# Kernel tuning notes

Measured on AMD Instinct MI355X. Metric: run time of the kernel, lower is better.

Reference implementation:

```python
import jax, jax.numpy as jnp
import numpy as np

N_ITER = 64   # projected-subgradient iterations of the batched DRO QP solver
LR0 = 0.05    # base step size (diminishing 1/sqrt(t))


def project_simplex(v):
    # Euclidean projection onto {z >= 0, sum z = 1} (sort-based, O(n log n))
    n = v.shape[0]
    u = jnp.sort(v)[::-1]
    css = jnp.cumsum(u) - 1.0
    k = jnp.arange(1, n + 1, dtype=v.dtype)
    cond = (u - css / k) > 0          # prefix-true pattern
    idx = jnp.sum(cond.astype(jnp.int32)) - 1
    theta = jnp.take(css, idx) / jnp.take(k, idx)
    return jnp.maximum(v - theta, 0.0)


def _dro_obj(z, c, lam, ep, y_hat, rho):
    # Tractable TV-DRO counterpart (Ben-Tal et al. 2013) with eta and obj_aux
    # eliminated analytically:
    #   obj_i* = max(-lam, u_i - eta),  u_i = (ep_i.z - c)^2
    #   feasibility: eta >= max_i u_i - lam; objective nondecreasing in eta
    #   => eta* = max_i u_i - lam
    s = ep @ z - c                     # (n_obs,)
    u = s * s
    umax = jnp.max(u)
    inner = jnp.mean(jnp.maximum(-lam, u - umax + lam))
    return (umax - lam) + rho * lam + inner - jnp.dot(y_hat, z)


_grad_obj = jax.grad(_dro_obj, argnums=(0, 1, 2))


def _solve_one(y_hat, ep, rho):
    # Projected subgradient descent on (z in simplex, c free, lam >= 0)
    n_y = y_hat.shape[0]
    z0 = jnp.full((n_y,), 1.0 / n_y, y_hat.dtype)
    c0 = jnp.mean(ep @ z0)
    lam0 = jnp.asarray(1.0, y_hat.dtype)

    def step(carry, t):
        z, c, lam = carry
        gz, gc, glam = _grad_obj(z, c, lam, ep, y_hat, rho)
        lr = LR0 / jnp.sqrt(t + 1.0)
        z = project_simplex(z - lr * gz)
        c = c - lr * gc
        lam = jnp.maximum(lam - lr * glam, 0.0)
        return (z, c, lam), None

    (z, _, _), _ = jax.lax.scan(step, (z0, c0, lam0),
                                jnp.arange(N_ITER, dtype=y_hat.dtype))
    return z


def setup_inputs() -> dict:
    key = jax.random.key(0)
    kx, ky, kw, kb = jax.random.split(key, 4)
    n_obs, n_x, n_y = 2048, 128, 64
    X = jax.random.normal(kx, (n_obs, n_x), jnp.float32)
    Y = jax.random.normal(ky, (n_obs, n_y), jnp.float32)
    W = jax.random.normal(kw, (n_y, n_x), jnp.float32) / np.sqrt(n_x).astype(np.float32)
    b = jax.random.normal(kb, (n_y,), jnp.float32) * 0.01
    rho = jnp.array([0.1], jnp.float32)
    return {"X": X, "Y": Y, "rho": rho, "W": W, "b": b}


def reference(X, Y, rho, W, b):
    # prediction layer: per-sample linear predict (vectorized over n_obs)
    Y_hat = X @ W.T + b                        # (n_obs, n_y)
    ep = Y - Y_hat                             # residuals, shared by all solves
    # batched DRO solve: one convex problem per scenario y_hat_t (vmapped)
    Z_star = jax.vmap(lambda yh: _solve_one(yh, ep, rho[0]))(Y_hat)
    Z_star = jax.lax.stop_gradient(Z_star)     # torch code detaches z_t
    return Z_star, Y_hat
```

## Files before the change

### kernel.cpp

```cpp
#include <hip/hip_runtime.h>

#define NOBS 2048
#define NX   128
#define NY   64
#define BS   8
#define NT   1024
#define NWAVE (NT / 64)
#define NITER 64

typedef short short8 __attribute__((ext_vector_type(8)));
typedef float f32x4 __attribute__((ext_vector_type(4)));

__device__ __forceinline__ unsigned short bf16_rne(float x) {
    unsigned u = __float_as_uint(x);
    return (unsigned short)((u + 0x7FFFu + ((u >> 16) & 1u)) >> 16);
}
__device__ __forceinline__ float bf16_tof(unsigned short h) {
    return __uint_as_float(((unsigned)h) << 16);
}

template <int CTRL>
__device__ __forceinline__ float dpp_f(float x) {
    return __int_as_float(__builtin_amdgcn_update_dpp(
        0, __float_as_int(x), CTRL, 0xf, 0xf, true));
}
__device__ __forceinline__ float wave_sum64(float v) {
    v += dpp_f<0x111>(v);
    v += dpp_f<0x112>(v);
    v += dpp_f<0x114>(v);
    v += dpp_f<0x118>(v);
    v += dpp_f<0x142>(v);
    v += dpp_f<0x143>(v);
    return v;
}
__device__ __forceinline__ float wave_max64_nonneg(float v) {
    v = fmaxf(v, dpp_f<0x111>(v));
    v = fmaxf(v, dpp_f<0x112>(v));
    v = fmaxf(v, dpp_f<0x114>(v));
    v = fmaxf(v, dpp_f<0x118>(v));
    v = fmaxf(v, dpp_f<0x142>(v));
    v = fmaxf(v, dpp_f<0x143>(v));
    return v;
}

__global__ __launch_bounds__(256) void prep_kernel(
    const float* __restrict__ X, const float* __restrict__ Y,
    const float* __restrict__ W, const float* __restrict__ b,
    float* __restrict__ yhat_out, float* __restrict__ ep, float* __restrict__ epsum,
    unsigned short* __restrict__ epT_hi, unsigned short* __restrict__ epT_lo)
{
    __shared__ float Xs[4][NX];
    const int t = threadIdx.x;
    const int row0 = blockIdx.x * 4;
    for (int f = t; f < 4 * NX; f += 256)
        Xs[f >> 7][f & 127] = X[(row0 + (f >> 7)) * NX + (f & 127)];
    __syncthreads();

    const int k = t & 63;
    const int r = t >> 6;
    const float4* W4 = reinterpret_cast<const float4*>(W + k * NX);
    const float4* X4 = reinterpret_cast<const float4*>(&Xs[r][0]);
    float acc = 0.f;
    #pragma unroll
    for (int x = 0; x < NX / 4; ++x) {
        float4 wv = W4[x];
        float4 xv = X4[x];
        acc += wv.x * xv.x + wv.y * xv.y + wv.z * xv.z + wv.w * xv.w;
    }
    const float yh = acc + b[k];
    const int i = row0 + r;
    yhat_out[i * NY + k] = yh;
    const float e = Y[i * NY + k] - yh;
    ep[i * NY + k] = e;

    {
        const unsigned short hi = bf16_rne(e);
        const unsigned short lo = bf16_rne(e - bf16_tof(hi));
        const int m  = k >> 4;
        const int q  = i >> 5;
        const int lc = (k & 15) + 16 * ((i >> 3) & 3);
        const int d  = i & 7;
        const int idx = ((m * 64 + q) * 64 + lc) * 8 + d;
        epT_hi[idx] = hi;
        epT_lo[idx] = lo;
    }

    float se = wave_sum64(e);
    if ((t & 63) == 63) atomicAdd(epsum, se);
}

__global__ __launch_bounds__(NT, 4) void solve_kernel(
    const float* __restrict__ ep, const float* __restrict__ yhat,
    const float* __restrict__ epsum, const float* __restrict__ rho_p,
    const unsigned short* __restrict__ epT_hi, const unsigned short* __restrict__ epT_lo,
    float* __restrict__ zout)
{
    __shared__ float Zs[BS][NY];
    __shared__ float Yh[BS][NY];
    __shared__ unsigned short VT_hi[BS][2056];
    __shared__ unsigned short VT_lo[BS][2056];
    __shared__ float Rp2[4][4][64][4];
    __shared__ float redM[NWAVE][BS];
    __shared__ float red2[NWAVE][4 * BS];
    __shared__ float cS[BS], lamS[BS];
    __shared__ __align__(16) unsigned short zb[8];

    const int t = threadIdx.x;
    const int lane = t & 63;
    const int wv = t >> 6;
    const int sc0 = blockIdx.x * BS;
    const float rho = rho_p[0];

    if (t < BS * NY) {
        const int j = t >> 6, k = t & 63;
        Yh[j][k] = yhat[(sc0 + j) * NY + k];
        Zs[j][k] = 1.0f / 64.0f;
    }
    if (t < BS) {
        cS[t] = epsum[0] * (1.0f / 131072.0f);
        lamS[t] = 1.0f;
    }
    if (t < 8) zb[t] = 0;
    __syncthreads();

    const int i0 = t;
    const int i1 = t + NT;
    const float4* ep4 = reinterpret_cast<const float4*>(ep);

    for (int it = 0; it < NITER; ++it) {
        const float lr = 0.05f / sqrtf((float)it + 1.0f);

        float s0[BS], s1[BS];
        #pragma unroll
        for (int j = 0; j < BS; ++j) { s0[j] = 0.f; s1[j] = 0.f; }
        #pragma unroll 4
        for (int k4 = 0; k4 < NY / 4; ++k4) {
            const float4 ea = ep4[i0 * (NY / 4) + k4];
            const float4 eb = ep4[i1 * (NY / 4) + k4];
            #pragma unroll
            for (int j = 0; j < BS; ++j) {
                const float4 zv = *reinterpret_cast<const float4*>(&Zs[j][k4 * 4]);
                s0[j] += ea.x * zv.x + ea.y * zv.y + ea.z * zv.z + ea.w * zv.w;
                s1[j] += eb.x * zv.x + eb.y * zv.y + eb.z * zv.z + eb.w * zv.w;
            }
        }
        float lamR[BS];
        #pragma unroll
        for (int j = 0; j < BS; ++j) {
            const float cj = cS[j];
            lamR[j] = lamS[j];
            s0[j] -= cj; s1[j] -= cj;
        }

        #pragma unroll
        for (int j = 0; j < BS; ++j) {
            float pm = fmaxf(s0[j] * s0[j], s1[j] * s1[j]);
            pm = wave_max64_nonneg(pm);
            if (lane == 63) redM[wv][j] = pm;
        }
        __syncthreads();

        float mv = 0.f;
        if (lane < BS) {
            #pragma unroll
            for (int w = 0; w < NWAVE; ++w) mv = fmaxf(mv, redM[w][lane]);
        }
        float umaxR[BS];
        #pragma unroll
        for (int j = 0; j < BS; ++j) umaxR[j] = __shfl(mv, j, 64);

        #pragma unroll
        for (int j = 0; j < BS; ++j) {
            const float um = umaxR[j], lm = lamR[j];
            float pa = 0.f, pe = 0.f, pas = 0.f, pes = 0.f;
            {
                const float s = s0[j], u = s * s;
                const float x = (u - um) + lm;
                const float a = (x > -lm) ? 1.0f : ((x == -lm) ? 0.5f : 0.0f);
                const float e = (u == um) ? 1.0f : 0.0f;
                pa += a; pe += e; pas += a * s; pes += e * s;
            }
            {
                const float s = s1[j], u = s * s;
                const float x = (u - um) + lm;
                const float a = (x > -lm) ? 1.0f : ((x == -lm) ? 0.5f : 0.0f);
                const float e = (u == um) ? 1.0f : 0.0f;
                pa += a; pe += e; pas += a * s; pes += e * s;
            }
            pa = wave_sum64(pa); pe = wave_sum64(pe);
            pas = wave_sum64(pas); pes = wave_sum64(pes);
            if (lane == 63) {
                red2[wv][j]          = pa;  red2[wv][BS + j]     = pe;
                red2[wv][2 * BS + j] = pas; red2[wv][3 * BS + j] = pes;
            }
        }
        __syncthreads();

        float sv = 0.f;
        if (lane < 4 * BS) {
            #pragma unroll
            for (int w = 0; w < NWAVE; ++w) sv += red2[w][lane];
        }
        float wAr[BS], gcKeep = 0.f, glamKeep = 0.f;
        #pragma unroll
        for (int j = 0; j < BS; ++j) {
            const float sumA   = __shfl(sv, j, 64);
            const float sumEq  = __shfl(sv, BS + j, 64);
            const float sumAS  = __shfl(sv, 2 * BS + j, 64);
            const float sumEqS = __shfl(sv, 3 * BS + j, 64);
            const float abar = sumA * (1.0f / (float)NOBS);
            const float wA = (1.0f - abar) / sumEq;
            wAr[j] = wA;
            if (lane == j) {
                gcKeep   = -2.0f * (sumAS * (1.0f / (float)NOBS) + wA * sumEqS);
                glamKeep = (rho - 2.0f) + 2.0f * abar;
            }
        }
        if (wv == 0 && lane < BS) {
            cS[lane]  = cS[lane] - lr * gcKeep;
            lamS[lane] = fmaxf(lamS[lane] - lr * glamKeep, 0.0f);
        }

        #pragma unroll
        for (int j = 0; j < BS; ++j) {
            const float um = umaxR[j], lm = lamR[j], wA = wAr[j];
            float v0j, v1j;
            {
                const float s = s0[j], u = s * s;
                const float x = (u - um) + lm;
                const float a = (x > -lm) ? 1.0f : ((x == -lm) ? 0.5f : 0.0f);
                const float e = (u == um) ? 1.0f : 0.0f;
                v0j = (a * (1.0f / (float)NOBS) + e * wA) * s;
            }
            {
                const float s = s1[j], u = s * s;
                const float x = (u - um) + lm;
                const float a = (x > -lm) ? 1.0f : ((x == -lm) ? 0.5f : 0.0f);
                const float e = (u == um) ? 1.0f : 0.0f;
                v1j = (a * (1.0f / (float)NOBS) + e * wA) * s;
            }
            const unsigned short h0 = bf16_rne(v0j);
            VT_hi[j][i0] = h0;
            VT_lo[j][i0] = bf16_rne(v0j - bf16_tof(h0));
            const unsigned short h1 = bf16_rne(v1j);
            VT_hi[j][i1] = h1;
            VT_lo[j][i1] = bf16_rne(v1j - bf16_tof(h1));
        }
        __syncthreads();

        {
            const int m = wv & 3;
            const int g = wv >> 2;
            const int jb = lane & 15;
            const int h  = lane >> 4;
            const bool jvalid = (jb < BS);
            f32x4 acc = {0.f, 0.f, 0.f, 0.f};
            #pragma unroll 4
            for (int qq = 0; qq < 16; ++qq) {
                const int q = g * 16 + qq;
                const int aoff = ((m * 64 + q) * 64 + lane) * 8;
                const short8 ah = *(const short8*)(epT_hi + aoff);
                const short8 al = *(const short8*)(epT_lo + aoff);
                const unsigned short* vh = jvalid ? &VT_hi[jb][(q << 5) + (h << 3)] : zb;
                const unsigned short* vl = jvalid ? &VT_lo[jb][(q << 5) + (h << 3)] : zb;
                const short8 bh = *(const short8*)vh;
                const short8 bl = *(const short8*)vl;
                acc = __builtin_amdgcn_mfma_f32_16x16x32_bf16(al, bh, acc, 0, 0, 0);
                acc = __builtin_amdgcn_mfma_f32_16x16x32_bf16(ah, bl, acc, 0, 0, 0);
                acc = __builtin_amdgcn_mfma_f32_16x16x32_bf16(ah, bh, acc, 0, 0, 0);
            }
            *(f32x4*)(&Rp2[g][m][lane][0]) = acc;
        }
        __syncthreads();

        if (wv < BS) {
            const int j = wv, k = lane;
            const int m = k >> 4, p = k & 3, ll = ((k >> 2) & 3) * 16 + j;
            const float r = Rp2[0][m][ll][p] + Rp2[1][m][ll][p]
                          + Rp2[2][m][ll][p] + Rp2[3][m][ll][p];
            const float gz = 2.0f * r - Yh[j][k];
            const float vz = Zs[j][k] - lr * gz;

            float sv2 = vz;
            #pragma unroll
            for (int sz = 2; sz <= 64; sz <<= 1) {
                #pragma unroll
                for (int st = sz >> 1; st > 0; st >>= 1) {
                    const float other = __shfl_xor(sv2, st, 64);
                    const bool desc = ((lane & sz) == 0);
                    const bool lower = ((lane & st) == 0);
                    const float mx = fmaxf(sv2, other), mn = fminf(sv2, other);
                    sv2 = (lower == desc) ? mx : mn;
                }
            }
            float css = sv2;
            #pragma unroll
            for (int off = 1; off < 64; off <<= 1) {
                const float nb = __shfl_up(css, off, 64);
                if (lane >= off) css += nb;
            }
            css -= 1.0f;
            const bool cond = (sv2 - css / (float)(lane + 1)) > 0.0f;
            const unsigned long long bal = __ballot(cond);
            const int idx = __popcll(bal) - 1;
            const float cssIdx = __shfl(css, idx, 64);
            const float theta = cssIdx / (float)(idx + 1);
            Zs[j][k] = fmaxf(vz - theta, 0.0f);
        }
        __syncthreads();
    }

    if (t < BS * NY) {
        const int j = t >> 6, k = t & 63;
        zout[(sc0 + j) * NY + k] = Zs[j][k];
    }
}

extern "C" void kernel_launch(void* const* d_in, const int* in_sizes, int n_in,
                              void* d_out, int out_size, void* d_ws, size_t ws_size,
                              hipStream_t stream) {
    const float* X   = (const float*)d_in[0];
    const float* Y   = (const float*)d_in[1];
    const float* rho = (const float*)d_in[2];
    const float* W   = (const float*)d_in[3];
    const float* b   = (const float*)d_in[4];

    float* out   = (float*)d_out;
    float* zout  = out;
    float* yhat  = out + NOBS * NY;

    unsigned short* epT_hi = (unsigned short*)d_ws;
    unsigned short* epT_lo = epT_hi + NY * NOBS;
    float* ep    = (float*)(epT_lo + NY * NOBS);
    float* epsum = ep + NOBS * NY;

    hipMemsetAsync(epsum, 0, sizeof(float), stream);
    prep_kernel<<<NOBS / 4, 256, 0, stream>>>(X, Y, W, b, yhat, ep, epsum, epT_hi, epT_lo);
    solve_kernel<<<NOBS / BS, NT, 0, stream>>>(ep, yhat, epsum, rho, epT_hi, epT_lo, zout);
}
```

Baseline: 1.892 ms.

## Compute forward residual products with triple-bf16 MFMA instead of scalar fp32 FMA

The forward product ep@z for all observations and 8 scenarios moves from scalar fp32 dot products over global float4 loads to bf16 MFMA. Residuals are split three ways (hi/md/lo) and z is split the same way, using six cross-term MFMAs to keep near-fp32 accuracy. The fp32 residual buffer goes away, and the reductions are reorganised around the MFMA output layout, using shuffles and vectorised VT writes. The cost is extra MFMA work on padded (duplicated) scenario columns, a third residual copy in memory, and a risk of small numerical drift that could change the argmax ties in the subgradient.

```diff
diff --git a/kernel.cpp b/kernel.cpp
--- a/kernel.cpp
+++ b/kernel.cpp
@@ -10,6 +10,7 @@
 
 typedef short short8 __attribute__((ext_vector_type(8)));
 typedef float f32x4 __attribute__((ext_vector_type(4)));
+typedef unsigned short u16x4 __attribute__((ext_vector_type(4)));
 
 __device__ __forceinline__ unsigned short bf16_rne(float x) {
     unsigned u = __float_as_uint(x);
@@ -33,21 +34,14 @@
     v += dpp_f<0x143>(v);
     return v;
 }
-__device__ __forceinline__ float wave_max64_nonneg(float v) {
-    v = fmaxf(v, dpp_f<0x111>(v));
-    v = fmaxf(v, dpp_f<0x112>(v));
-    v = fmaxf(v, dpp_f<0x114>(v));
-    v = fmaxf(v, dpp_f<0x118>(v));
-    v = fmaxf(v, dpp_f<0x142>(v));
-    v = fmaxf(v, dpp_f<0x143>(v));
-    return v;
-}
 
 __global__ __launch_bounds__(256) void prep_kernel(
     const float* __restrict__ X, const float* __restrict__ Y,
     const float* __restrict__ W, const float* __restrict__ b,
-    float* __restrict__ yhat_out, float* __restrict__ ep, float* __restrict__ epsum,
-    unsigned short* __restrict__ epT_hi, unsigned short* __restrict__ epT_lo)
+    float* __restrict__ yhat_out, float* __restrict__ epsum,
+    unsigned short* __restrict__ epT_hi, unsigned short* __restrict__ epT_lo,
+    unsigned short* __restrict__ epA_hi, unsigned short* __restrict__ epA_md,
+    unsigned short* __restrict__ epA_lo)
 {
     __shared__ float Xs[4][NX];
     const int t = threadIdx.x;
@@ -71,18 +65,29 @@
     const int i = row0 + r;
     yhat_out[i * NY + k] = yh;
     const float e = Y[i * NY + k] - yh;
-    ep[i * NY + k] = e;
-
+
+    const unsigned short hi = bf16_rne(e);
+    const float r1 = e - bf16_tof(hi);
+    const unsigned short md = bf16_rne(r1);
+    const unsigned short lo = bf16_rne(r1 - bf16_tof(md));
     {
-        const unsigned short hi = bf16_rne(e);
-        const unsigned short lo = bf16_rne(e - bf16_tof(hi));
         const int m  = k >> 4;
         const int q  = i >> 5;
         const int lc = (k & 15) + 16 * ((i >> 3) & 3);
         const int d  = i & 7;
         const int idx = ((m * 64 + q) * 64 + lc) * 8 + d;
         epT_hi[idx] = hi;
-        epT_lo[idx] = lo;
+        epT_lo[idx] = md;
+    }
+    {
+        const int m  = i >> 4;
+        const int q  = k >> 5;
+        const int lc = (i & 15) + 16 * ((k >> 3) & 3);
+        const int d  = k & 7;
+        const int idx = ((m * 2 + q) * 64 + lc) * 8 + d;
+        epA_hi[idx] = hi;
+        epA_md[idx] = md;
+        epA_lo[idx] = lo;
     }
 
     float se = wave_sum64(e);
@@ -90,24 +95,33 @@
 }
 
 __global__ __launch_bounds__(NT, 4) void solve_kernel(
-    const float* __restrict__ ep, const float* __restrict__ yhat,
-    const float* __restrict__ epsum, const float* __restrict__ rho_p,
+    const float* __restrict__ yhat, const float* __restrict__ epsum,
+    const float* __restrict__ rho_p,
     const unsigned short* __restrict__ epT_hi, const unsigned short* __restrict__ epT_lo,
+    const unsigned short* __restrict__ epA_hi, const unsigned short* __restrict__ epA_md,
+    const unsigned short* __restrict__ epA_lo,
     float* __restrict__ zout)
 {
     __shared__ float Zs[BS][NY];
     __shared__ float Yh[BS][NY];
     __shared__ unsigned short VT_hi[BS][2056];
     __shared__ unsigned short VT_lo[BS][2056];
+    __shared__ __align__(16) unsigned short Zb_hi[16][72];
+    __shared__ __align__(16) unsigned short Zb_md[16][72];
+    __shared__ __align__(16) unsigned short Zb_lo[16][72];
     __shared__ float Rp2[4][4][64][4];
     __shared__ float redM[NWAVE][BS];
-    __shared__ float red2[NWAVE][4 * BS];
-    __shared__ float cS[BS], lamS[BS];
+    __shared__ float red2[NWAVE][BS][4];
+    __shared__ float cS[16], lamS[16];
     __shared__ __align__(16) unsigned short zb[8];
 
     const int t = threadIdx.x;
     const int lane = t & 63;
     const int wv = t >> 6;
+    const int jb = lane & 15;
+    const int h  = lane >> 4;
+    const int j8 = jb & 7;
+    const bool hiHalf = (jb >= 8);
     const int sc0 = blockIdx.x * BS;
     const float rho = rho_p[0];
 
@@ -116,160 +130,147 @@
         Yh[j][k] = yhat[(sc0 + j) * NY + k];
         Zs[j][k] = 1.0f / 64.0f;
     }
-    if (t < BS) {
+    {
+        const int j = t >> 6, k = t & 63;
+        Zb_hi[j][k] = bf16_rne(1.0f / 64.0f);
+        Zb_md[j][k] = 0;
+        Zb_lo[j][k] = 0;
+    }
+    if (t < 16) {
         cS[t] = epsum[0] * (1.0f / 131072.0f);
         lamS[t] = 1.0f;
     }
     if (t < 8) zb[t] = 0;
     __syncthreads();
 
-    const int i0 = t;
-    const int i1 = t + NT;
-    const float4* ep4 = reinterpret_cast<const float4*>(ep);
-
     for (int it = 0; it < NITER; ++it) {
         const float lr = 0.05f / sqrtf((float)it + 1.0f);
 
-        float s0[BS], s1[BS];
-        #pragma unroll
-        for (int j = 0; j < BS; ++j) { s0[j] = 0.f; s1[j] = 0.f; }
-        #pragma unroll 4
-        for (int k4 = 0; k4 < NY / 4; ++k4) {
-            const float4 ea = ep4[i0 * (NY / 4) + k4];
-            const float4 eb = ep4[i1 * (NY / 4) + k4];
-            #pragma unroll
-            for (int j = 0; j < BS; ++j) {
-                const float4 zv = *reinterpret_cast<const float4*>(&Zs[j][k4 * 4]);
-                s0[j] += ea.x * zv.x + ea.y * zv.y + ea.z * zv.z + ea.w * zv.w;
-                s1[j] += eb.x * zv.x + eb.y * zv.y + eb.z * zv.z + eb.w * zv.w;
-            }
-        }
-        float lamR[BS];
-        #pragma unroll
-        for (int j = 0; j < BS; ++j) {
-            const float cj = cS[j];
-            lamR[j] = lamS[j];
-            s0[j] -= cj; s1[j] -= cj;
-        }
-
-        #pragma unroll
-        for (int j = 0; j < BS; ++j) {
-            float pm = fmaxf(s0[j] * s0[j], s1[j] * s1[j]);
-            pm = wave_max64_nonneg(pm);
-            if (lane == 63) redM[wv][j] = pm;
-        }
-        __syncthreads();
-
-        float mv = 0.f;
-        if (lane < BS) {
-            #pragma unroll
-            for (int w = 0; w < NWAVE; ++w) mv = fmaxf(mv, redM[w][lane]);
-        }
-        float umaxR[BS];
-        #pragma unroll
-        for (int j = 0; j < BS; ++j) umaxR[j] = __shfl(mv, j, 64);
-
-        #pragma unroll
-        for (int j = 0; j < BS; ++j) {
-            const float um = umaxR[j], lm = lamR[j];
-            float pa = 0.f, pe = 0.f, pas = 0.f, pes = 0.f;
-            {
-                const float s = s0[j], u = s * s;
+        f32x4 acc[8];
+        #pragma unroll
+        for (int mi = 0; mi < 8; ++mi) acc[mi] = (f32x4){0.f, 0.f, 0.f, 0.f};
+        #pragma unroll
+        for (int q = 0; q < 2; ++q) {
+            const short8 zh = *(const short8*)&Zb_hi[jb][(q << 5) + (h << 3)];
+            const short8 zm = *(const short8*)&Zb_md[jb][(q << 5) + (h << 3)];
+            const short8 zl = *(const short8*)&Zb_lo[jb][(q << 5) + (h << 3)];
+            #pragma unroll
+            for (int mi = 0; mi < 8; ++mi) {
+                const int aoff = ((((wv << 3) + mi) * 2 + q) * 64 + lane) * 8;
+                const short8 ah = *(const short8*)(epA_hi + aoff);
+                const short8 am = *(const short8*)(epA_md + aoff);
+                const short8 al = *(const short8*)(epA_lo + aoff);
+                acc[mi] = __builtin_amdgcn_mfma_f32_16x16x32_bf16(al, zh, acc[mi], 0, 0, 0);
+                acc[mi] = __builtin_amdgcn_mfma_f32_16x16x32_bf16(ah, zl, acc[mi], 0, 0, 0);
+                acc[mi] = __builtin_amdgcn_mfma_f32_16x16x32_bf16(am, zm, acc[mi], 0, 0, 0);
+                acc[mi] = __builtin_amdgcn_mfma_f32_16x16x32_bf16(am, zh, acc[mi], 0, 0, 0);
+                acc[mi] = __builtin_amdgcn_mfma_f32_16x16x32_bf16(ah, zm, acc[mi], 0, 0, 0);
+                acc[mi] = __builtin_amdgcn_mfma_f32_16x16x32_bf16(ah, zh, acc[mi], 0, 0, 0);
+            }
+        }
+        const float cR = cS[jb];
+        const float lm = lamS[jb];
+        float sv_[4][4], u_[4][4];
+        #pragma unroll
+        for (int n = 0; n < 4; ++n)
+            #pragma unroll
+            for (int p = 0; p < 4; ++p) {
+                const float av = hiHalf ? acc[n + 4][p] : acc[n][p];
+                const float ss = av - cR;
+                sv_[n][p] = ss;
+                u_[n][p] = ss * ss;
+            }
+
+        float pm = u_[0][0];
+        #pragma unroll
+        for (int n = 0; n < 4; ++n)
+            #pragma unroll
+            for (int p = 0; p < 4; ++p) pm = fmaxf(pm, u_[n][p]);
+        pm = fmaxf(pm, __shfl_xor(pm, 8, 64));
+        pm = fmaxf(pm, __shfl_xor(pm, 16, 64));
+        pm = fmaxf(pm, __shfl_xor(pm, 32, 64));
+        if (lane < 8) redM[wv][lane] = pm;
+        __syncthreads();
+
+        float um = redM[0][j8];
+        #pragma unroll
+        for (int w = 1; w < NWAVE; ++w) um = fmaxf(um, redM[w][j8]);
+
+        float pa = 0.f, pe = 0.f, pas = 0.f, pes = 0.f;
+        #pragma unroll
+        for (int n = 0; n < 4; ++n)
+            #pragma unroll
+            for (int p = 0; p < 4; ++p) {
+                const float ss = sv_[n][p], u = u_[n][p];
                 const float x = (u - um) + lm;
                 const float a = (x > -lm) ? 1.0f : ((x == -lm) ? 0.5f : 0.0f);
                 const float e = (u == um) ? 1.0f : 0.0f;
-                pa += a; pe += e; pas += a * s; pes += e * s;
-            }
-            {
-                const float s = s1[j], u = s * s;
+                pa += a; pe += e; pas += a * ss; pes += e * ss;
+            }
+        pa  += __shfl_xor(pa, 8, 64);  pa  += __shfl_xor(pa, 16, 64);  pa  += __shfl_xor(pa, 32, 64);
+        pe  += __shfl_xor(pe, 8, 64);  pe  += __shfl_xor(pe, 16, 64);  pe  += __shfl_xor(pe, 32, 64);
+        pas += __shfl_xor(pas, 8, 64); pas += __shfl_xor(pas, 16, 64); pas += __shfl_xor(pas, 32, 64);
+        pes += __shfl_xor(pes, 8, 64); pes += __shfl_xor(pes, 16, 64); pes += __shfl_xor(pes, 32, 64);
+        if (lane < 8) {
+            f32x4 r4 = {pa, pe, pas, pes};
+            *(f32x4*)&red2[wv][lane][0] = r4;
+        }
+        __syncthreads();
+
+        float sA = 0.f, sE = 0.f, sAS = 0.f, sES = 0.f;
+        #pragma unroll
+        for (int w = 0; w < NWAVE; ++w) {
+            const f32x4 rr = *(const f32x4*)&red2[w][j8][0];
+            sA += rr[0]; sE += rr[1]; sAS += rr[2]; sES += rr[3];
+        }
+        const float abar = sA * (1.0f / (float)NOBS);
+        const float wA = (1.0f - abar) / sE;
+        const float gc = -2.0f * (sAS * (1.0f / (float)NOBS) + wA * sES);
+        const float glam = (rho - 2.0f) + 2.0f * abar;
+        if (wv == 0 && lane < 16) {
+            cS[lane] = cS[lane] - lr * gc;
+            lamS[lane] = fmaxf(lamS[lane] - lr * glam, 0.0f);
+        }
+
+        #pragma unroll
+        for (int n = 0; n < 4; ++n) {
+            u16x4 vh4, vl4;
+            #pragma unroll
+            for (int p = 0; p < 4; ++p) {
+                const float ss = sv_[n][p], u = u_[n][p];
                 const float x = (u - um) + lm;
                 const float a = (x > -lm) ? 1.0f : ((x == -lm) ? 0.5f : 0.0f);
                 const float e = (u == um) ? 1.0f : 0.0f;
-                pa += a; pe += e; pas += a * s; pes += e * s;
-            }
-            pa = wave_sum64(pa); pe = wave_sum64(pe);
-            pas = wave_sum64(pas); pes = wave_sum64(pes);
-            if (lane == 63) {
-                red2[wv][j]          = pa;  red2[wv][BS + j]     = pe;
-                red2[wv][2 * BS + j] = pas; red2[wv][3 * BS + j] = pes;
-            }
-        }
-        __syncthreads();
-
-        float sv = 0.f;
-        if (lane < 4 * BS) {
-            #pragma unroll
-            for (int w = 0; w < NWAVE; ++w) sv += red2[w][lane];
-        }
-        float wAr[BS], gcKeep = 0.f, glamKeep = 0.f;
-        #pragma unroll
-        for (int j = 0; j < BS; ++j) {
-            const float sumA   = __shfl(sv, j, 64);
-            const float sumEq  = __shfl(sv, BS + j, 64);
-            const float sumAS  = __shfl(sv, 2 * BS + j, 64);
-            const float sumEqS = __shfl(sv, 3 * BS + j, 64);
-            const float abar = sumA * (1.0f / (float)NOBS);
-            const float wA = (1.0f - abar) / sumEq;
-            wAr[j] = wA;
-            if (lane == j) {
-                gcKeep   = -2.0f * (sumAS * (1.0f / (float)NOBS) + wA * sumEqS);
-                glamKeep = (rho - 2.0f) + 2.0f * abar;
-            }
-        }
-        if (wv == 0 && lane < BS) {
-            cS[lane]  = cS[lane] - lr * gcKeep;
-            lamS[lane] = fmaxf(lamS[lane] - lr * glamKeep, 0.0f);
-        }
-
-        #pragma unroll
-        for (int j = 0; j < BS; ++j) {
-            const float um = umaxR[j], lm = lamR[j], wA = wAr[j];
-            float v0j, v1j;
-            {
-                const float s = s0[j], u = s * s;
-                const float x = (u - um) + lm;
-                const float a = (x > -lm) ? 1.0f : ((x == -lm) ? 0.5f : 0.0f);
-                const float e = (u == um) ? 1.0f : 0.0f;
-                v0j = (a * (1.0f / (float)NOBS) + e * wA) * s;
-            }
-            {
-                const float s = s1[j], u = s * s;
-                const float x = (u - um) + lm;
-                const float a = (x > -lm) ? 1.0f : ((x == -lm) ? 0.5f : 0.0f);
-                const float e = (u == um) ? 1.0f : 0.0f;
-                v1j = (a * (1.0f / (float)NOBS) + e * wA) * s;
-            }
-            const unsigned short h0 = bf16_rne(v0j);
-            VT_hi[j][i0] = h0;
-            VT_lo[j][i0] = bf16_rne(v0j - bf16_tof(h0));
-            const unsigned short h1 = bf16_rne(v1j);
-            VT_hi[j][i1] = h1;
-            VT_lo[j][i1] = bf16_rne(v1j - bf16_tof(h1));
+                const float vv = (a * (1.0f / (float)NOBS) + e * wA) * ss;
+                const unsigned short vhh = bf16_rne(vv);
+                vh4[p] = vhh;
+                vl4[p] = bf16_rne(vv - bf16_tof(vhh));
+            }
+            const int ii = ((wv << 3) + (hiHalf ? 4 : 0) + n) * 16 + (h << 2);
+            *(u16x4*)&VT_hi[j8][ii] = vh4;
+            *(u16x4*)&VT_lo[j8][ii] = vl4;
         }
         __syncthreads();
 
         {
             const int m = wv & 3;
             const int g = wv >> 2;
-            const int jb = lane & 15;
-            const int h  = lane >> 4;
-            const bool jvalid = (jb < BS);
-            f32x4 acc = {0.f, 0.f, 0.f, 0.f};
+            f32x4 accC = {0.f, 0.f, 0.f, 0.f};
             #pragma unroll 4
             for (int qq = 0; qq < 16; ++qq) {
                 const int q = g * 16 + qq;
                 const int aoff = ((m * 64 + q) * 64 + lane) * 8;
                 const short8 ah = *(const short8*)(epT_hi + aoff);
                 const short8 al = *(const short8*)(epT_lo + aoff);
-                const unsigned short* vh = jvalid ? &VT_hi[jb][(q << 5) + (h << 3)] : zb;
-                const unsigned short* vl = jvalid ? &VT_lo[jb][(q << 5) + (h << 3)] : zb;
+                const unsigned short* vh = (!hiHalf) ? &VT_hi[jb][(q << 5) + (h << 3)] : zb;
+                const unsigned short* vl = (!hiHalf) ? &VT_lo[jb][(q << 5) + (h << 3)] : zb;
                 const short8 bh = *(const short8*)vh;
                 const short8 bl = *(const short8*)vl;
-                acc = __builtin_amdgcn_mfma_f32_16x16x32_bf16(al, bh, acc, 0, 0, 0);
-                acc = __builtin_amdgcn_mfma_f32_16x16x32_bf16(ah, bl, acc, 0, 0, 0);
-                acc = __builtin_amdgcn_mfma_f32_16x16x32_bf16(ah, bh, acc, 0, 0, 0);
-            }
-            *(f32x4*)(&Rp2[g][m][lane][0]) = acc;
+                accC = __builtin_amdgcn_mfma_f32_16x16x32_bf16(al, bh, accC, 0, 0, 0);
+                accC = __builtin_amdgcn_mfma_f32_16x16x32_bf16(ah, bl, accC, 0, 0, 0);
+                accC = __builtin_amdgcn_mfma_f32_16x16x32_bf16(ah, bh, accC, 0, 0, 0);
+            }
+            *(f32x4*)(&Rp2[g][m][lane][0]) = accC;
         }
         __syncthreads();
 
@@ -305,7 +306,15 @@
             const int idx = __popcll(bal) - 1;
             const float cssIdx = __shfl(css, idx, 64);
             const float theta = cssIdx / (float)(idx + 1);
-            Zs[j][k] = fmaxf(vz - theta, 0.0f);
+            const float zk = fmaxf(vz - theta, 0.0f);
+            Zs[j][k] = zk;
+            const unsigned short zh_ = bf16_rne(zk);
+            const float zr1 = zk - bf16_tof(zh_);
+            const unsigned short zm_ = bf16_rne(zr1);
+            const unsigned short zl_ = bf16_rne(zr1 - bf16_tof(zm_));
+            Zb_hi[j][k] = zh_; Zb_hi[j + 8][k] = zh_;
+            Zb_md[j][k] = zm_; Zb_md[j + 8][k] = zm_;
+            Zb_lo[j][k] = zl_; Zb_lo[j + 8][k] = zl_;
         }
         __syncthreads();
     }
@@ -331,10 +340,14 @@
 
     unsigned short* epT_hi = (unsigned short*)d_ws;
     unsigned short* epT_lo = epT_hi + NY * NOBS;
-    float* ep    = (float*)(epT_lo + NY * NOBS);
-    float* epsum = ep + NOBS * NY;
+    unsigned short* epA_hi = epT_lo + NY * NOBS;
+    unsigned short* epA_md = epA_hi + NY * NOBS;
+    unsigned short* epA_lo = epA_md + NY * NOBS;
+    float* epsum = (float*)(epA_lo + NY * NOBS);
 
     hipMemsetAsync(epsum, 0, sizeof(float), stream);
-    prep_kernel<<<NOBS / 4, 256, 0, stream>>>(X, Y, W, b, yhat, ep, epsum, epT_hi, epT_lo);
-    solve_kernel<<<NOBS / BS, NT, 0, stream>>>(ep, yhat, epsum, rho, epT_hi, epT_lo, zout);
-}
+    prep_kernel<<<NOBS / 4, 256, 0, stream>>>(X, Y, W, b, yhat, epsum,
+                                              epT_hi, epT_lo, epA_hi, epA_md, epA_lo);
+    solve_kernel<<<NOBS / BS, NT, 0, stream>>>(yhat, epsum, rho,
+                                               epT_hi, epT_lo, epA_hi, epA_md, epA_lo, zout);
+}
```

New measurement: 3.286 ms. 73.7% more time.
